# Optimization experiments

Hardware: AMD Instinct MI355X
Metric: run time of the kernel (lower is better)

## Reference

```python
import jax, jax.numpy as jnp
import numpy as np

NUM_HEADS = 2
D = 512
D_HID = 2048


def _layer_norm(x, g, b, eps):
    mu = jnp.mean(x, axis=-1, keepdims=True)
    var = jnp.var(x, axis=-1, keepdims=True)
    return (x - mu) * jax.lax.rsqrt(var + eps) * g + b


def _attn_block(Q, K, V, resnet, Wq, Wk, Wv, ln_g, ln_b, w1, w2, fln_g, fln_b):
    # Linear projections (torch Linear: x @ W.T), no bias
    q = Q @ Wq.T
    k = K @ Wk.T
    v = V @ Wv.T
    B, N, C = q.shape
    gs = C // NUM_HEADS  # group size per head
    # split channels into heads == reshape [B,N,H,gs] -> [B,H,N,gs]
    qh = q.reshape(B, N, NUM_HEADS, gs).transpose(0, 2, 1, 3)
    kh = k.reshape(B, K.shape[1], NUM_HEADS, gs).transpose(0, 2, 1, 3)
    vh = v.reshape(B, V.shape[1], NUM_HEADS, gs).transpose(0, 2, 1, 3)
    scores = jnp.einsum('bhqd,bhkd->bhqk', qh, kh) / jnp.sqrt(jnp.asarray(gs, q.dtype))
    attn = jax.nn.softmax(scores, axis=-1)
    out = jnp.einsum('bhqk,bhkd->bhqd', attn, vh)
    # concat heads back to channel dim
    out = out.transpose(0, 2, 1, 3).reshape(B, N, C)
    x = out + resnet
    x = _layer_norm(x, ln_g, ln_b, 1e-5)
    # FFN (dropout is identity in eval mode)
    residual = x
    y = jax.nn.relu(x @ w1.T) @ w2.T
    y = y + residual
    y = _layer_norm(y, fln_g, fln_b, 1e-6)
    return y


def setup_inputs() -> dict:
    key = jax.random.key(0)
    ks = jax.random.split(key, 16)
    B, N = 4, 2048
    Fm = jax.random.normal(ks[0], (B, N, D), dtype=jnp.float32)
    Fs = jax.random.normal(ks[1], (B, N, D), dtype=jnp.float32)
    Fq = jax.random.normal(ks[2], (B, N, D), dtype=jnp.float32)
    s = 0.02
    Wq = jax.random.normal(ks[3], (3, D, D), dtype=jnp.float32) * s
    Wk = jax.random.normal(ks[4], (3, D, D), dtype=jnp.float32) * s
    Wv = jax.random.normal(ks[5], (3, D, D), dtype=jnp.float32) * s
    ln_g = jnp.ones((3, D), dtype=jnp.float32)
    ln_b = jnp.zeros((3, D), dtype=jnp.float32)
    w1 = jax.random.normal(ks[6], (3, D_HID, D), dtype=jnp.float32) * s
    w2 = jax.random.normal(ks[7], (3, D, D_HID), dtype=jnp.float32) * s
    fln_g = jnp.ones((3, D), dtype=jnp.float32)
    fln_b = jnp.zeros((3, D), dtype=jnp.float32)
    return {"Fm": Fm, "Fs": Fs, "Fq": Fq, "Wq": Wq, "Wk": Wk, "Wv": Wv,
            "ln_g": ln_g, "ln_b": ln_b, "w1": w1, "w2": w2,
            "fln_g": fln_g, "fln_b": fln_b, "out_dim": 512}


def reference(Fm, Fs, Fq, Wq, Wk, Wv, ln_g, ln_b, w1, w2, fln_g, fln_b, out_dim):
    def blk(i, Q, K, V, resnet):
        return _attn_block(Q, K, V, resnet, Wq[i], Wk[i], Wv[i], ln_g[i], ln_b[i],
                           w1[i], w2[i], fln_g[i], fln_b[i])
    css = blk(0, Fs, Fs, Fm, Fm)
    cqq = blk(1, Fq, Fq, Fq, Fq)
    csq = blk(2, cqq, Fs, css, css)
    return csq
```

## Files before the change

kernel.cpp:

```cpp
#include <hip/hip_runtime.h>

typedef __bf16 bf16_t;
typedef __bf16 bf16x8 __attribute__((ext_vector_type(8)));
typedef __bf16 bf16x4 __attribute__((ext_vector_type(4)));
typedef float  f32x4  __attribute__((ext_vector_type(4)));

#define GAS __attribute__((address_space(1)))
#define LAS __attribute__((address_space(3)))

enum { EPI_BF16 = 0, EPI_RELU = 1 };

struct GPtrs {
    const bf16_t* A[6];
    const bf16_t* B[6];
    bf16_t*       C[6];
};

__global__ void probe_dtype(const unsigned* __restrict__ lng_bits, int* __restrict__ flag)
{
    *flag = (lng_bits[0] == 0x3F800000u) ? 0 : 1;
}

__global__ __launch_bounds__(256) void conv_any3(
    const void* __restrict__ s0, const void* __restrict__ s1, const void* __restrict__ s2,
    bf16_t* __restrict__ d0, bf16_t* __restrict__ d1, bf16_t* __restrict__ d2,
    const int* __restrict__ flag, int n8)
{
    int i = blockIdx.x * 256 + threadIdx.x;
    if (i >= n8) return;
    const void* src = (blockIdx.z == 0) ? s0 : (blockIdx.z == 1) ? s1 : s2;
    bf16_t*    dst = (blockIdx.z == 0) ? d0 : (blockIdx.z == 1) ? d1 : d2;
    if (*flag == 0) {
        const float4* s = (const float4*)src;
        float4 a = s[i * 2], b = s[i * 2 + 1];
        bf16x8 o = { (bf16_t)a.x, (bf16_t)a.y, (bf16_t)a.z, (bf16_t)a.w,
                     (bf16_t)b.x, (bf16_t)b.y, (bf16_t)b.z, (bf16_t)b.w };
        ((bf16x8*)dst)[i] = o;
    } else {
        ((uint4*)dst)[i] = ((const uint4*)src)[i];
    }
}

__global__ __launch_bounds__(256) void widen_ln4(
    const void* __restrict__ a, const void* __restrict__ b,
    const void* __restrict__ c, const void* __restrict__ d,
    float* __restrict__ dst, const int* __restrict__ flag, int n)
{
    int i = blockIdx.x * 256 + threadIdx.x;
    int seg = i / n, j = i - seg * n;
    if (seg >= 4) return;
    const void* s = (seg == 0) ? a : (seg == 1) ? b : (seg == 2) ? c : d;
    dst[i] = (*flag == 0) ? ((const float*)s)[j]
                          : (float)((const bf16_t*)s)[j];
}

template<int EPI, int TMv, int TNv, int WM, int WN, bool TABLE, int ZH, bool VT>
__global__ __launch_bounds__(WM * WN * 64, (WM * WN == 8) ? 4 : 2) void gemm_bt(
    GPtrs P, int K, int lda, int ldb, int ldc,
    long sAb, long sAh, long sBb, long sBh, long sCb, long sCh,
    float scale)
{
    constexpr int THREADS = WM * WN * 64;
    constexpr int MF = TMv / WM / 16, NF = TNv / WN / 16;
    constexpr int STG = 2 * (TMv + TNv) * 32;
    constexpr int RPK = TMv * TNv;
    constexpr int SME = (STG > RPK) ? STG : RPK;
    __shared__ __align__(16) bf16_t smem[SME];
    bf16_t* Asb = smem;
    bf16_t* Bsb = smem + 2 * TMv * 32;

    const int z = blockIdx.z;
    const bf16_t* A; const bf16_t* B; bf16_t* C; long cOff = 0;
    if constexpr (TABLE) {
        A = P.A[z]; B = P.B[z]; C = P.C[z];
    } else {
        const int half = z / ZH, zz = z % ZH;
        const long zb = zz >> 1, zh = zz & 1;
        A = P.A[half] + zb * sAb + zh * sAh;
        B = P.B[half] + zb * sBb + zh * sBh;
        C = P.C[half]; cOff = zb * sCb + zh * sCh;
    }

    int m_t, n_t;
    {
        const int gx = gridDim.x, gy = gridDim.y;
        if ((gy & 7) == 0) {
            const int L = blockIdx.y * gx + blockIdx.x;
            const int band_h = gy >> 3;
            const int r = L >> 3;
            m_t = (L & 7) * band_h + (r % band_h);
            n_t = r / band_h;
        } else { m_t = blockIdx.y; n_t = blockIdx.x; }
    }
    const int n0 = n_t * TNv;
    const int m0 = m_t * TMv;

    const int tid  = threadIdx.x;
    const int wave = tid >> 6, lane = tid & 63;
    const int wm = (wave / WN) * (TMv / WM);
    const int wn = (wave % WN) * (TNv / WN);
    const int lrow = lane & 15, lquad = lane >> 4;
    const int rq   = (lquad ^ ((lrow >> 1) & 3)) * 8;
    const int srow0 = tid >> 2;
    const int scol0 = ((tid & 3) ^ ((tid >> 3) & 3)) * 8;
    constexpr int ITA = (TMv * 4) / THREADS;
    constexpr int ITB = (TNv * 4) / THREADS;
    constexpr int RSW = THREADS / 4;

    f32x4 acc[MF][NF];
    #pragma unroll
    for (int i = 0; i < MF; i++)
        #pragma unroll
        for (int j = 0; j < NF; j++) acc[i][j] = (f32x4){0.f, 0.f, 0.f, 0.f};

    const bf16_t* aP = A + (long)(m0 + srow0) * lda + scol0;
    const bf16_t* bP = B + (long)(n0 + srow0) * ldb + scol0;
    const int wbase = wave * 64 * 8;

    for (int kk = 0; kk < K; kk += 64) {
        __syncthreads();
        #pragma unroll
        for (int p = 0; p < 2; p++) {
            #pragma unroll
            for (int i = 0; i < ITA; i++)
                __builtin_amdgcn_global_load_lds(
                    (GAS void*)(aP + p * 32 + (long)i * RSW * lda),
                    (LAS void*)(Asb + p * TMv * 32 + i * THREADS * 8 + wbase), 16, 0, 0);
            #pragma unroll
            for (int i = 0; i < ITB; i++)
                __builtin_amdgcn_global_load_lds(
                    (GAS void*)(bP + p * 32 + (long)i * RSW * ldb),
                    (LAS void*)(Bsb + p * TNv * 32 + i * THREADS * 8 + wbase), 16, 0, 0);
        }
        aP += 64; bP += 64;
        __syncthreads();

        #pragma unroll
        for (int p = 0; p < 2; p++) {
            bf16x8 af[MF], bfr[NF];
            #pragma unroll
            for (int mi = 0; mi < MF; mi++)
                af[mi] = *(const bf16x8*)&Asb[(p * TMv + wm + mi * 16 + lrow) * 32 + rq];
            #pragma unroll
            for (int ni = 0; ni < NF; ni++)
                bfr[ni] = *(const bf16x8*)&Bsb[(p * TNv + wn + ni * 16 + lrow) * 32 + rq];
            #pragma unroll
            for (int mi = 0; mi < MF; mi++)
                #pragma unroll
                for (int ni = 0; ni < NF; ni++)
                    acc[mi][ni] = __builtin_amdgcn_mfma_f32_16x16x32_bf16(
                        af[mi], bfr[ni], acc[mi][ni], 0, 0, 0);
        }
    }

    if (VT && (z % 3 == 2)) {
        #pragma unroll
        for (int mi = 0; mi < MF; mi++)
            #pragma unroll
            for (int ni = 0; ni < NF; ni++) {
                const int mr = m0 + wm + mi * 16 + lquad * 4;
                const int nc = n0 + wn + ni * 16 + lrow;
                const int b = mr >> 11, s = mr & 2047;
                const int h = nc >> 8,  d = nc & 255;
                bf16x4 t = { (bf16_t)(acc[mi][ni][0]),
                             (bf16_t)(acc[mi][ni][1]),
                             (bf16_t)(acc[mi][ni][2]),
                             (bf16_t)(acc[mi][ni][3]) };
                *(bf16x4*)&C[(((long)(b * 2 + h) * 256 + d) << 11) + s] = t;
            }
        return;
    }

    __syncthreads();
    #pragma unroll
    for (int mi = 0; mi < MF; mi++)
        #pragma unroll
        for (int ni = 0; ni < NF; ni++)
            #pragma unroll
            for (int r = 0; r < 4; r++) {
                float v = acc[mi][ni][r] * scale;
                if (EPI == EPI_RELU) v = fmaxf(v, 0.f);
                const int rI = wm + mi * 16 + lquad * 4 + r;
                const int c  = wn + ni * 16 + lrow;
                const int cs = c ^ (((((rI >> 2) & 3) ^ (rI & 3))) << 4);
                smem[rI * TNv + cs] = (bf16_t)v;
            }
    __syncthreads();
    constexpr int TPR = TNv / 8;
    constexpr int RPP = THREADS / TPR;
    const int srow = tid / TPR;
    const int scol = (tid % TPR) * 8;
    #pragma unroll
    for (int pass = 0; pass < TMv / RPP; pass++) {
        const int rr = pass * RPP + srow;
        const int cc = scol ^ (((((rr >> 2) & 3) ^ (rr & 3))) << 4);
        bf16x8 vv = *(const bf16x8*)&smem[rr * TNv + cc];
        *(bf16x8*)&C[cOff + (long)(m0 + rr) * ldc + n0 + scol] = vv;
    }
}

__global__ __launch_bounds__(256) void softmax_rows(bf16_t* __restrict__ buf)
{
    const long base = (long)blockIdx.x * 2048;
    const int tid = threadIdx.x;
    const int wave = tid >> 6, lane = tid & 63;
    __shared__ float red[8];
    bf16x8 x = *(const bf16x8*)&buf[base + tid * 8];
    float v[8];
    float mx = -1e30f;
    #pragma unroll
    for (int j = 0; j < 8; j++) { v[j] = (float)x[j]; mx = fmaxf(mx, v[j]); }
    for (int off = 32; off; off >>= 1) mx = fmaxf(mx, __shfl_xor(mx, off));
    if (lane == 0) red[wave] = mx;
    __syncthreads();
    mx = fmaxf(fmaxf(red[0], red[1]), fmaxf(red[2], red[3]));
    float s = 0.f;
    #pragma unroll
    for (int j = 0; j < 8; j++) { v[j] = __expf(v[j] - mx); s += v[j]; }
    for (int off = 32; off; off >>= 1) s += __shfl_xor(s, off);
    if (lane == 0) red[4 + wave] = s;
    __syncthreads();
    s = red[4] + red[5] + red[6] + red[7];
    const float inv = 1.f / s;
    bf16x8 y;
    #pragma unroll
    for (int j = 0; j < 8; j++) y[j] = (bf16_t)(v[j] * inv);
    *(bf16x8*)&buf[base + tid * 8] = y;
}

__global__ __launch_bounds__(256) void add_ln2(
    const bf16_t* xA, const bf16_t* rA, const float* gA, const float* bA, bf16_t* oA,
    const bf16_t* xB, const bf16_t* rB, const float* gB, const float* bB, bf16_t* oB,
    float eps, int splitRows)
{
    const int wave = threadIdx.x >> 6, lane = threadIdx.x & 63;
    long row = (long)blockIdx.x * 4 + wave;
    const bf16_t* xin; const bf16_t* res; const float* g; const float* bias; bf16_t* out;
    if (row >= splitRows) {
        row -= splitRows;
        xin = xB; res = rB; g = gB; bias = bB; out = oB;
    } else {
        xin = xA; res = rA; g = gA; bias = bA; out = oA;
    }
    const long base = row * 512 + lane * 8;
    bf16x8 a8 = *(const bf16x8*)&xin[base];
    bf16x8 r8 = *(const bf16x8*)&res[base];
    float v[8];
    #pragma unroll
    for (int j = 0; j < 8; j++) v[j] = (float)a8[j] + (float)r8[j];
    float s = 0.f, s2 = 0.f;
    #pragma unroll
    for (int j = 0; j < 8; j++) { s += v[j]; s2 += v[j] * v[j]; }
    for (int off = 32; off; off >>= 1) { s += __shfl_xor(s, off); s2 += __shfl_xor(s2, off); }
    const float mu  = s * (1.f / 512.f);
    const float var = s2 * (1.f / 512.f) - mu * mu;
    const float rs  = rsqrtf(var + eps);
    const int c0 = lane * 8;
    float4 g0 = *(const float4*)&g[c0];
    float4 g1 = *(const float4*)&g[c0 + 4];
    float4 b0 = *(const float4*)&bias[c0];
    float4 b1 = *(const float4*)&bias[c0 + 4];
    float gv[8] = { g0.x, g0.y, g0.z, g0.w, g1.x, g1.y, g1.z, g1.w };
    float bv[8] = { b0.x, b0.y, b0.z, b0.w, b1.x, b1.y, b1.z, b1.w };
    #pragma unroll
    for (int j = 0; j < 8; j++)
        out[base + j] = (bf16_t)((v[j] - mu) * rs * gv[j] + bv[j]);
}

__global__ __launch_bounds__(256) void add_ln_f32(
    const bf16_t* xin, const bf16_t* __restrict__ res,
    const float* __restrict__ g, const float* __restrict__ bias,
    float* out, float eps)
{
    const int wave = threadIdx.x >> 6, lane = threadIdx.x & 63;
    const long row = (long)blockIdx.x * 4 + wave;
    const long base = row * 512 + lane * 8;
    bf16x8 a8 = *(const bf16x8*)&xin[base];
    bf16x8 r8 = *(const bf16x8*)&res[base];
    float v[8];
    #pragma unroll
    for (int j = 0; j < 8; j++) v[j] = (float)a8[j] + (float)r8[j];
    float s = 0.f, s2 = 0.f;
    #pragma unroll
    for (int j = 0; j < 8; j++) { s += v[j]; s2 += v[j] * v[j]; }
    for (int off = 32; off; off >>= 1) { s += __shfl_xor(s, off); s2 += __shfl_xor(s2, off); }
    const float mu  = s * (1.f / 512.f);
    const float var = s2 * (1.f / 512.f) - mu * mu;
    const float rs  = rsqrtf(var + eps);
    const int c0 = lane * 8;
    float4 g0 = *(const float4*)&g[c0];
    float4 g1 = *(const float4*)&g[c0 + 4];
    float4 b0 = *(const float4*)&bias[c0];
    float4 b1 = *(const float4*)&bias[c0 + 4];
    float gv[8] = { g0.x, g0.y, g0.z, g0.w, g1.x, g1.y, g1.z, g1.w };
    float bv[8] = { b0.x, b0.y, b0.z, b0.w, b1.x, b1.y, b1.z, b1.w };
    #pragma unroll
    for (int j = 0; j < 8; j++)
        out[base + j] = (v[j] - mu) * rs * gv[j] + bv[j];
}

extern "C" void kernel_launch(void* const* d_in, const int* in_sizes, int n_in,
                              void* d_out, int out_size, void* d_ws, size_t ws_size,
                              hipStream_t stream)
{
    const void* Fm    = d_in[0];
    const void* Fs    = d_in[1];
    const void* Fq    = d_in[2];
    const void* Wq    = d_in[3];
    const void* Wk    = d_in[4];
    const void* Wv    = d_in[5];
    const void* ln_g  = d_in[6];
    const void* ln_b  = d_in[7];
    const void* w1    = d_in[8];
    const void* w2    = d_in[9];
    const void* fln_g = d_in[10];
    const void* fln_b = d_in[11];
    (void)in_sizes; (void)n_in; (void)out_size; (void)ws_size;

    char* ws = (char*)d_ws;
    size_t off = 0;
    auto take = [&](size_t bytes) {
        char* p = ws + off;
        off += (bytes + 255) & ~(size_t)255;
        return p;
    };
    const size_t NT = 8192ul * 512;

    int*    flag = (int*)take(256);
    float*  lnw  = (float*)take(4ul * 1536 * 4);
    bf16_t* Fm_b = (bf16_t*)take(NT * 2);
    bf16_t* Fs_b = (bf16_t*)take(NT * 2);
    bf16_t* Fq_b = (bf16_t*)take(NT * 2);
    bf16_t* wqb  = (bf16_t*)take(3ul * 512 * 512 * 2);
    bf16_t* wkb  = (bf16_t*)take(3ul * 512 * 512 * 2);
    bf16_t* wvb  = (bf16_t*)take(3ul * 512 * 512 * 2);
    bf16_t* w1b  = (bf16_t*)take(3ul * 2048 * 512 * 2);
    bf16_t* w2b  = (bf16_t*)take(3ul * 512 * 2048 * 2);
    bf16_t* q0   = (bf16_t*)take(NT * 2);
    bf16_t* k0   = (bf16_t*)take(NT * 2);
    bf16_t* q1   = (bf16_t*)take(NT * 2);
    bf16_t* k1   = (bf16_t*)take(NT * 2);
    bf16_t* vT0  = (bf16_t*)take(NT * 2);
    bf16_t* vT1  = (bf16_t*)take(NT * 2);
    bf16_t* scb  = (bf16_t*)take(2ul * 8 * 2048 * 2048 * 2);

    bf16_t* sc0 = scb;
    bf16_t* sc1 = scb + 8ul * 2048 * 2048;
    bf16_t* ao0 = q0;  bf16_t* ao1 = q1;
    bf16_t* x0  = k0;  bf16_t* x1  = k1;
    bf16_t* h0  = scb; bf16_t* h1  = scb + 16ul * 1024 * 1024;
    bf16_t* y0  = vT0; bf16_t* y1  = vT1;
    bf16_t* css = Fm_b;
    bf16_t* cqq = Fq_b;
    bf16_t* q2  = q0;  bf16_t* k2  = k0;  bf16_t* vT2 = vT0;
    bf16_t* sc2 = scb; bf16_t* ao2 = q1;  bf16_t* x2  = k1;
    bf16_t* h2  = scb + 32ul * 1024 * 1024;  bf16_t* y2 = vT1;

    dim3 blk(256), blk8(512);
    probe_dtype<<<dim3(1), dim3(1), 0, stream>>>((const unsigned*)ln_g, flag);

    conv_any3<<<dim3(2048, 1, 3), blk, 0, stream>>>(
        Fm, Fs, Fq, Fm_b, Fs_b, Fq_b, flag, (int)(NT / 8));
    conv_any3<<<dim3(384, 1, 3), blk, 0, stream>>>(
        Wq, Wk, Wv, wqb, wkb, wvb, flag, (int)(3ul * 512 * 512 / 8));
    conv_any3<<<dim3(1536, 1, 2), blk, 0, stream>>>(
        w1, w2, w2, w1b, w2b, w2b, flag, (int)(3ul * 2048 * 512 / 8));
    widen_ln4<<<dim3(24), blk, 0, stream>>>(ln_g, ln_b, fln_g, fln_b, lnw, flag, 1536);

    auto W  = [&](bf16_t* base, int i, size_t n) { return (const bf16_t*)(base + (size_t)i * n); };
    const float* g1[3]; const float* b1[3]; const float* g2[3]; const float* b2[3];
    for (int i = 0; i < 3; i++) {
        g1[i] = lnw + i * 512;            b1[i] = lnw + 1536 + i * 512;
        g2[i] = lnw + 2 * 1536 + i * 512; b2[i] = lnw + 3 * 1536 + i * 512;
    }

    {
        GPtrs P{};
        P.A[0] = Fs_b; P.A[1] = Fs_b; P.A[2] = Fm_b;
        P.A[3] = Fq_b; P.A[4] = Fq_b; P.A[5] = Fq_b;
        P.B[0] = W(wqb, 0, 512*512); P.B[1] = W(wkb, 0, 512*512); P.B[2] = W(wvb, 0, 512*512);
        P.B[3] = W(wqb, 1, 512*512); P.B[4] = W(wkb, 1, 512*512); P.B[5] = W(wvb, 1, 512*512);
        P.C[0] = q0; P.C[1] = k0; P.C[2] = vT0;
        P.C[3] = q1; P.C[4] = k1; P.C[5] = vT1;
        gemm_bt<EPI_BF16, 128, 128, 2, 2, true, 1, true><<<dim3(4, 64, 6), blk, 0, stream>>>(
            P, 512, 512, 512, 512, 0, 0, 0, 0, 0, 0, 1.f);
    }
    {
        GPtrs P{}; P.A[0] = q0; P.A[1] = q1; P.B[0] = k0; P.B[1] = k1;
        P.C[0] = sc0; P.C[1] = sc1;
        gemm_bt<EPI_BF16, 128, 128, 2, 2, false, 8, false><<<dim3(16, 16, 16), blk, 0, stream>>>(
            P, 256, 512, 512, 2048,
            1048576L, 256L, 1048576L, 256L, 8388608L, 4194304L, 0.0625f);
    }
    softmax_rows<<<dim3(32768), blk, 0, stream>>>(scb);
    {
        GPtrs P{}; P.A[0] = sc0; P.A[1] = sc1; P.B[0] = vT0; P.B[1] = vT1;
        P.C[0] = ao0; P.C[1] = ao1;
        gemm_bt<EPI_BF16, 128, 128, 2, 4, false, 8, false><<<dim3(2, 16, 16), blk8, 0, stream>>>(
            P, 2048, 2048, 2048, 512,
            8388608L, 4194304L, 1048576L, 524288L, 1048576L, 256L, 1.f);
    }
    add_ln2<<<dim3(4096), blk, 0, stream>>>(
        ao0, Fm_b, g1[0], b1[0], x0,
        ao1, Fq_b, g1[1], b1[1], x1, 1e-5f, 8192);
    {
        GPtrs P{}; P.A[0] = x0; P.A[1] = x1;
        P.B[0] = W(w1b, 0, 2048*512); P.B[1] = W(w1b, 1, 2048*512);
        P.C[0] = h0; P.C[1] = h1;
        gemm_bt<EPI_RELU, 128, 128, 2, 2, false, 1, false><<<dim3(16, 64, 2), blk, 0, stream>>>(
            P, 512, 512, 512, 2048, 0, 0, 0, 0, 0, 0, 1.f);
    }
    {
        GPtrs P{}; P.A[0] = h0; P.A[1] = h1;
        P.B[0] = W(w2b, 0, 512*2048); P.B[1] = W(w2b, 1, 512*2048);
        P.C[0] = y0; P.C[1] = y1;
        gemm_bt<EPI_BF16, 128, 128, 2, 4, false, 1, false><<<dim3(4, 64, 2), blk8, 0, stream>>>(
            P, 2048, 2048, 2048, 512, 0, 0, 0, 0, 0, 0, 1.f);
    }
    add_ln2<<<dim3(4096), blk, 0, stream>>>(
        y0, x0, g2[0], b2[0], css,
        y1, x1, g2[1], b2[1], cqq, 1e-6f, 8192);

    {
        GPtrs P{};
        P.A[0] = cqq; P.A[1] = Fs_b; P.A[2] = css;
        P.B[0] = W(wqb, 2, 512*512); P.B[1] = W(wkb, 2, 512*512); P.B[2] = W(wvb, 2, 512*512);
        P.C[0] = q2; P.C[1] = k2; P.C[2] = vT2;
        gemm_bt<EPI_BF16, 128, 128, 2, 2, true, 1, true><<<dim3(4, 64, 3), blk, 0, stream>>>(
            P, 512, 512, 512, 512, 0, 0, 0, 0, 0, 0, 1.f);
    }
    {
        GPtrs P{}; P.A[0] = q2; P.B[0] = k2; P.C[0] = sc2;
        gemm_bt<EPI_BF16, 128, 128, 2, 2, false, 8, false><<<dim3(16, 16, 8), blk, 0, stream>>>(
            P, 256, 512, 512, 2048,
            1048576L, 256L, 1048576L, 256L, 8388608L, 4194304L, 0.0625f);
    }
    softmax_rows<<<dim3(16384), blk, 0, stream>>>(sc2);
    {
        GPtrs P{}; P.A[0] = sc2; P.B[0] = vT2; P.C[0] = ao2;
        gemm_bt<EPI_BF16, 128, 128, 2, 4, false, 8, false><<<dim3(2, 16, 8), blk8, 0, stream>>>(
            P, 2048, 2048, 2048, 512,
            8388608L, 4194304L, 1048576L, 524288L, 1048576L, 256L, 1.f);
    }
    add_ln2<<<dim3(2048), blk, 0, stream>>>(
        ao2, css, g1[2], b1[2], x2,
        ao2, css, g1[2], b1[2], x2, 1e-5f, 1 << 30);
    {
        GPtrs P{}; P.A[0] = x2; P.B[0] = W(w1b, 2, 2048*512); P.C[0] = h2;
        gemm_bt<EPI_RELU, 128, 128, 2, 2, false, 1, false><<<dim3(16, 64, 1), blk, 0, stream>>>(
            P, 512, 512, 512, 2048, 0, 0, 0, 0, 0, 0, 1.f);
    }
    {
        GPtrs P{}; P.A[0] = h2; P.B[0] = W(w2b, 2, 512*2048); P.C[0] = y2;
        gemm_bt<EPI_BF16, 128, 128, 2, 4, false, 1, false><<<dim3(4, 64, 1), blk8, 0, stream>>>(
            P, 2048, 2048, 2048, 512, 0, 0, 0, 0, 0, 0, 1.f);
    }
    add_ln_f32<<<dim3(2048), blk, 0, stream>>>(
        y2, x2, g2[2], b2[2], (float*)d_out, 1e-6f);
}
```

Before: 585.9 us.

## Fuse softmax into QK and PV GEMMs via partial row statistics

Removes the standalone softmax pass, which read and rewrote the full score matrix. The QK^T GEMM epilogue now emits per-tile row max and exp-sum partials, a small kernel merges them into a global max and inverse sum per row, and the PV GEMM exponentiates and normalizes the raw scores as it loads A fragments. This saves one read and one write of the large bf16 score buffer. In exchange the PV kernel does exp work inside its inner loop, which is repeated for each N-tile, and two small stats buffers are added.

```diff
diff --git a/kernel.cpp b/kernel.cpp
--- a/kernel.cpp
+++ b/kernel.cpp
@@ -54,9 +54,11 @@
                           : (float)((const bf16_t*)s)[j];
 }
 
-template<int EPI, int TMv, int TNv, int WM, int WN, bool TABLE, int ZH, bool VT>
+template<int EPI, int TMv, int TNv, int WM, int WN, bool TABLE, int ZH, bool VT,
+         bool STATS, bool PVEXP>
 __global__ __launch_bounds__(WM * WN * 64, (WM * WN == 8) ? 4 : 2) void gemm_bt(
-    GPtrs P, int K, int lda, int ldb, int ldc,
+    GPtrs P, float2* __restrict__ SP, const float2* __restrict__ MS,
+    int K, int lda, int ldb, int ldc,
     long sAb, long sAh, long sBb, long sBh, long sCb, long sCh,
     float scale)
 {
@@ -107,6 +109,15 @@
     constexpr int ITB = (TNv * 4) / THREADS;
     constexpr int RSW = THREADS / 4;
 
+    float mrow[MF], ilrow[MF];
+    if constexpr (PVEXP) {
+        #pragma unroll
+        for (int mi = 0; mi < MF; mi++) {
+            float2 st = MS[(long)z * 2048 + m0 + wm + mi * 16 + lrow];
+            mrow[mi] = st.x; ilrow[mi] = st.y;
+        }
+    }
+
     f32x4 acc[MF][NF];
     #pragma unroll
     for (int i = 0; i < MF; i++)
@@ -141,6 +152,18 @@
             #pragma unroll
             for (int mi = 0; mi < MF; mi++)
                 af[mi] = *(const bf16x8*)&Asb[(p * TMv + wm + mi * 16 + lrow) * 32 + rq];
+            if constexpr (PVEXP) {
+                #pragma unroll
+                for (int mi = 0; mi < MF; mi++) {
+                    bf16x8 pa;
+                    #pragma unroll
+                    for (int e = 0; e < 8; e++) {
+                        float fe = (float)af[mi][e];
+                        pa[e] = (bf16_t)(__expf(fe - mrow[mi]) * ilrow[mi]);
+                    }
+                    af[mi] = pa;
+                }
+            }
             #pragma unroll
             for (int ni = 0; ni < NF; ni++)
                 bfr[ni] = *(const bf16x8*)&Bsb[(p * TNv + wn + ni * 16 + lrow) * 32 + rq];
@@ -169,6 +192,34 @@
                 *(bf16x4*)&C[(((long)(b * 2 + h) * 256 + d) << 11) + s] = t;
             }
         return;
+    }
+
+    if constexpr (STATS) {
+        const int entry = n_t * 2 + (wn >> 6);
+        #pragma unroll
+        for (int mi = 0; mi < MF; mi++)
+            #pragma unroll
+            for (int r = 0; r < 4; r++) {
+                float vb[NF];
+                float mt = -1e30f;
+                #pragma unroll
+                for (int ni = 0; ni < NF; ni++) {
+                    vb[ni] = (float)(bf16_t)(acc[mi][ni][r] * scale);
+                    mt = fmaxf(mt, vb[ni]);
+                }
+                #pragma unroll
+                for (int off = 1; off < 16; off <<= 1)
+                    mt = fmaxf(mt, __shfl_xor(mt, off));
+                float se = 0.f;
+                #pragma unroll
+                for (int ni = 0; ni < NF; ni++) se += __expf(vb[ni] - mt);
+                #pragma unroll
+                for (int off = 1; off < 16; off <<= 1) se += __shfl_xor(se, off);
+                if ((lane & 15) == 0) {
+                    const long rw = (long)z * 2048 + m0 + wm + mi * 16 + lquad * 4 + r;
+                    SP[rw * 32 + entry] = (float2){mt, se};
+                }
+            }
     }
 
     __syncthreads();
@@ -199,33 +250,19 @@
     }
 }
 
-__global__ __launch_bounds__(256) void softmax_rows(bf16_t* __restrict__ buf)
-{
-    const long base = (long)blockIdx.x * 2048;
-    const int tid = threadIdx.x;
-    const int wave = tid >> 6, lane = tid & 63;
-    __shared__ float red[8];
-    bf16x8 x = *(const bf16x8*)&buf[base + tid * 8];
-    float v[8];
-    float mx = -1e30f;
-    #pragma unroll
-    for (int j = 0; j < 8; j++) { v[j] = (float)x[j]; mx = fmaxf(mx, v[j]); }
-    for (int off = 32; off; off >>= 1) mx = fmaxf(mx, __shfl_xor(mx, off));
-    if (lane == 0) red[wave] = mx;
-    __syncthreads();
-    mx = fmaxf(fmaxf(red[0], red[1]), fmaxf(red[2], red[3]));
-    float s = 0.f;
-    #pragma unroll
-    for (int j = 0; j < 8; j++) { v[j] = __expf(v[j] - mx); s += v[j]; }
-    for (int off = 32; off; off >>= 1) s += __shfl_xor(s, off);
-    if (lane == 0) red[4 + wave] = s;
-    __syncthreads();
-    s = red[4] + red[5] + red[6] + red[7];
-    const float inv = 1.f / s;
-    bf16x8 y;
-    #pragma unroll
-    for (int j = 0; j < 8; j++) y[j] = (bf16_t)(v[j] * inv);
-    *(bf16x8*)&buf[base + tid * 8] = y;
+__global__ __launch_bounds__(256) void combine_stats(
+    const float2* __restrict__ sp, float2* __restrict__ ms, int nrows)
+{
+    const int wave = threadIdx.x >> 6, lane = threadIdx.x & 63;
+    const int row = blockIdx.x * 4 + wave;
+    if (row >= nrows) return;
+    float m = -1e30f, l = 0.f;
+    if (lane < 32) { float2 s = sp[(long)row * 32 + lane]; m = s.x; l = s.y; }
+    float gm = m;
+    for (int off = 32; off; off >>= 1) gm = fmaxf(gm, __shfl_xor(gm, off));
+    float t = l * __expf(m - gm);
+    for (int off = 32; off; off >>= 1) t += __shfl_xor(t, off);
+    if (lane == 0) ms[row] = (float2){gm, 1.f / t};
 }
 
 __global__ __launch_bounds__(256) void add_ln2(
@@ -328,6 +365,8 @@
 
     int*    flag = (int*)take(256);
     float*  lnw  = (float*)take(4ul * 1536 * 4);
+    float2* statsP = (float2*)take(16ul * 2048 * 32 * 8);
+    float2* mstats = (float2*)take(16ul * 2048 * 8);
     bf16_t* Fm_b = (bf16_t*)take(NT * 2);
     bf16_t* Fs_b = (bf16_t*)take(NT * 2);
     bf16_t* Fq_b = (bf16_t*)take(NT * 2);
@@ -382,22 +421,25 @@
         P.B[3] = W(wqb, 1, 512*512); P.B[4] = W(wkb, 1, 512*512); P.B[5] = W(wvb, 1, 512*512);
         P.C[0] = q0; P.C[1] = k0; P.C[2] = vT0;
         P.C[3] = q1; P.C[4] = k1; P.C[5] = vT1;
-        gemm_bt<EPI_BF16, 128, 128, 2, 2, true, 1, true><<<dim3(4, 64, 6), blk, 0, stream>>>(
-            P, 512, 512, 512, 512, 0, 0, 0, 0, 0, 0, 1.f);
+        gemm_bt<EPI_BF16, 128, 128, 2, 2, true, 1, true, false, false>
+            <<<dim3(4, 64, 6), blk, 0, stream>>>(
+            P, nullptr, nullptr, 512, 512, 512, 512, 0, 0, 0, 0, 0, 0, 1.f);
     }
     {
         GPtrs P{}; P.A[0] = q0; P.A[1] = q1; P.B[0] = k0; P.B[1] = k1;
         P.C[0] = sc0; P.C[1] = sc1;
-        gemm_bt<EPI_BF16, 128, 128, 2, 2, false, 8, false><<<dim3(16, 16, 16), blk, 0, stream>>>(
-            P, 256, 512, 512, 2048,
+        gemm_bt<EPI_BF16, 128, 128, 2, 2, false, 8, false, true, false>
+            <<<dim3(16, 16, 16), blk, 0, stream>>>(
+            P, statsP, nullptr, 256, 512, 512, 2048,
             1048576L, 256L, 1048576L, 256L, 8388608L, 4194304L, 0.0625f);
     }
-    softmax_rows<<<dim3(32768), blk, 0, stream>>>(scb);
+    combine_stats<<<dim3(8192), blk, 0, stream>>>(statsP, mstats, 32768);
     {
         GPtrs P{}; P.A[0] = sc0; P.A[1] = sc1; P.B[0] = vT0; P.B[1] = vT1;
         P.C[0] = ao0; P.C[1] = ao1;
-        gemm_bt<EPI_BF16, 128, 128, 2, 4, false, 8, false><<<dim3(2, 16, 16), blk8, 0, stream>>>(
-            P, 2048, 2048, 2048, 512,
+        gemm_bt<EPI_BF16, 128, 128, 2, 4, false, 8, false, false, true>
+            <<<dim3(2, 16, 16), blk8, 0, stream>>>(
+            P, nullptr, mstats, 2048, 2048, 2048, 512,
             8388608L, 4194304L, 1048576L, 524288L, 1048576L, 256L, 1.f);
     }
     add_ln2<<<dim3(4096), blk, 0, stream>>>(
@@ -407,15 +449,17 @@
         GPtrs P{}; P.A[0] = x0; P.A[1] = x1;
         P.B[0] = W(w1b, 0, 2048*512); P.B[1] = W(w1b, 1, 2048*512);
         P.C[0] = h0; P.C[1] = h1;
-        gemm_bt<EPI_RELU, 128, 128, 2, 2, false, 1, false><<<dim3(16, 64, 2), blk, 0, stream>>>(
-            P, 512, 512, 512, 2048, 0, 0, 0, 0, 0, 0, 1.f);
+        gemm_bt<EPI_RELU, 128, 128, 2, 2, false, 1, false, false, false>
+            <<<dim3(16, 64, 2), blk, 0, stream>>>(
+            P, nullptr, nullptr, 512, 512, 512, 2048, 0, 0, 0, 0, 0, 0, 1.f);
     }
     {
         GPtrs P{}; P.A[0] = h0; P.A[1] = h1;
         P.B[0] = W(w2b, 0, 512*2048); P.B[1] = W(w2b, 1, 512*2048);
         P.C[0] = y0; P.C[1] = y1;
-        gemm_bt<EPI_BF16, 128, 128, 2, 4, false, 1, false><<<dim3(4, 64, 2), blk8, 0, stream>>>(
-            P, 2048, 2048, 2048, 512, 0, 0, 0, 0, 0, 0, 1.f);
+        gemm_bt<EPI_BF16, 128, 128, 2, 4, false, 1, false, false, false>
+            <<<dim3(4, 64, 2), blk8, 0, stream>>>(
+            P, nullptr, nullptr, 2048, 2048, 2048, 512, 0, 0, 0, 0, 0, 0, 1.f);
     }
     add_ln2<<<dim3(4096), blk, 0, stream>>>(
         y0, x0, g2[0], b2[0], css,
@@ -426,20 +470,23 @@
         P.A[0] = cqq; P.A[1] = Fs_b; P.A[2] = css;
         P.B[0] = W(wqb, 2, 512*512); P.B[1] = W(wkb, 2, 512*512); P.B[2] = W(wvb, 2, 512*512);
         P.C[0] = q2; P.C[1] = k2; P.C[2] = vT2;
-        gemm_bt<EPI_BF16, 128, 128, 2, 2, true, 1, true><<<dim3(4, 64, 3), blk, 0, stream>>>(
-            P, 512, 512, 512, 512, 0, 0, 0, 0, 0, 0, 1.f);
+        gemm_bt<EPI_BF16, 128, 128, 2, 2, true, 1, true, false, false>
+            <<<dim3(4, 64, 3), blk, 0, stream>>>(
+            P, nullptr, nullptr, 512, 512, 512, 512, 0, 0, 0, 0, 0, 0, 1.f);
     }
     {
         GPtrs P{}; P.A[0] = q2; P.B[0] = k2; P.C[0] = sc2;
-        gemm_bt<EPI_BF16, 128, 128, 2, 2, false, 8, false><<<dim3(16, 16, 8), blk, 0, stream>>>(
-            P, 256, 512, 512, 2048,
+        gemm_bt<EPI_BF16, 128, 128, 2, 2, false, 8, false, true, false>
+            <<<dim3(16, 16, 8), blk, 0, stream>>>(
+            P, statsP, nullptr, 256, 512, 512, 2048,
             1048576L, 256L, 1048576L, 256L, 8388608L, 4194304L, 0.0625f);
     }
-    softmax_rows<<<dim3(16384), blk, 0, stream>>>(sc2);
+    combine_stats<<<dim3(4096), blk, 0, stream>>>(statsP, mstats, 16384);
     {
         GPtrs P{}; P.A[0] = sc2; P.B[0] = vT2; P.C[0] = ao2;
-        gemm_bt<EPI_BF16, 128, 128, 2, 4, false, 8, false><<<dim3(2, 16, 8), blk8, 0, stream>>>(
-            P, 2048, 2048, 2048, 512,
+        gemm_bt<EPI_BF16, 128, 128, 2, 4, false, 8, false, false, true>
+            <<<dim3(2, 16, 8), blk8, 0, stream>>>(
+            P, nullptr, mstats, 2048, 2048, 2048, 512,
             8388608L, 4194304L, 1048576L, 524288L, 1048576L, 256L, 1.f);
     }
     add_ln2<<<dim3(2048), blk, 0, stream>>>(
@@ -447,13 +494,15 @@
         ao2, css, g1[2], b1[2], x2, 1e-5f, 1 << 30);
     {
         GPtrs P{}; P.A[0] = x2; P.B[0] = W(w1b, 2, 2048*512); P.C[0] = h2;
-        gemm_bt<EPI_RELU, 128, 128, 2, 2, false, 1, false><<<dim3(16, 64, 1), blk, 0, stream>>>(
-            P, 512, 512, 512, 2048, 0, 0, 0, 0, 0, 0, 1.f);
+        gemm_bt<EPI_RELU, 128, 128, 2, 2, false, 1, false, false, false>
+            <<<dim3(16, 64, 1), blk, 0, stream>>>(
+            P, nullptr, nullptr, 512, 512, 512, 2048, 0, 0, 0, 0, 0, 0, 1.f);
     }
     {
         GPtrs P{}; P.A[0] = h2; P.B[0] = W(w2b, 2, 512*2048); P.C[0] = y2;
-        gemm_bt<EPI_BF16, 128, 128, 2, 4, false, 1, false><<<dim3(4, 64, 1), blk8, 0, stream>>>(
-            P, 2048, 2048, 2048, 512, 0, 0, 0, 0, 0, 0, 1.f);
+        gemm_bt<EPI_BF16, 128, 128, 2, 4, false, 1, false, false, false>
+            <<<dim3(4, 64, 1), blk8, 0, stream>>>(
+            P, nullptr, nullptr, 2048, 2048, 2048, 512, 0, 0, 0, 0, 0, 0, 1.f);
     }
     add_ln_f32<<<dim3(2048), blk, 0, stream>>>(
         y2, x2, g2[2], b2[2], (float*)d_out, 1e-6f);
```

Measured after the change: 697.0 us. 19.0% more time.
